# Kernel tuning notes

Measured on AMD Instinct MI355X. Metric: run time of the kernel, lower is better.

The kernel has to match this reference:

```python
import jax, jax.numpy as jnp
import numpy as np

EPS = 1e-5
NHEAD = 8
TOP_K = 2


def _layernorm(x, g, b):
    m = jnp.mean(x, axis=-1, keepdims=True)
    v = jnp.mean((x - m) ** 2, axis=-1, keepdims=True)
    return (x - m) * jax.lax.rsqrt(v + EPS) * g + b


def setup_inputs() -> dict:
    S, D, F, E = 4096, 512, 2048, 8
    key = jax.random.key(0)
    ks = jax.random.split(key, 18)
    std = 0.02
    return {
        "src": jax.random.normal(ks[0], (S, D), jnp.float32),
        "in_proj_w": std * jax.random.normal(ks[1], (3 * D, D), jnp.float32),
        "in_proj_b": jnp.zeros((3 * D,), jnp.float32),
        "out_proj_w": std * jax.random.normal(ks[2], (D, D), jnp.float32),
        "out_proj_b": jnp.zeros((D,), jnp.float32),
        "ln1_g": jnp.ones((D,), jnp.float32),
        "ln1_b": jnp.zeros((D,), jnp.float32),
        "ln2_g": jnp.ones((D,), jnp.float32),
        "ln2_b": jnp.zeros((D,), jnp.float32),
        "gate_w": std * jax.random.normal(ks[3], (E, D), jnp.float32),
        "gate_b": jnp.zeros((E,), jnp.float32),
        "w1": std * jax.random.normal(ks[4], (E, F, D), jnp.float32),
        "b1": jnp.zeros((E, F), jnp.float32),
        "w2": std * jax.random.normal(ks[5], (E, F, D), jnp.float32),
        "b2": jnp.zeros((E, F), jnp.float32),
        "wo": std * jax.random.normal(ks[6], (E, D, F), jnp.float32),
        "bo": jnp.zeros((E, D), jnp.float32),
    }


def _sa_block(x, in_proj_w, in_proj_b, out_proj_w, out_proj_b):
    # x: [S, D] unbatched sequence (torch MultiheadAttention unbatched path)
    S, D = x.shape
    hd = D // NHEAD
    qkv = x @ in_proj_w.T + in_proj_b              # [S, 3D]
    q, k, v = jnp.split(qkv, 3, axis=-1)
    q = q.reshape(S, NHEAD, hd)
    k = k.reshape(S, NHEAD, hd)
    v = v.reshape(S, NHEAD, hd)
    scores = jnp.einsum("shd,thd->hst", q, k) / jnp.sqrt(jnp.float32(hd))
    attn = jax.nn.softmax(scores, axis=-1)         # [H, S, S]
    out = jnp.einsum("hst,thd->shd", attn, v).reshape(S, D)
    return out @ out_proj_w.T + out_proj_b


def _ff_block(x, gate_w, gate_b, w1, b1, w2, b2, wo, bo):
    # top-k gated SwiGLU MoE; gate probs are softmax, NOT renormalized after topk
    T = x.shape[0]
    E = w1.shape[0]
    gates = jax.nn.softmax(x @ gate_w.T + gate_b, axis=-1)      # [T, E]
    top_scores, top_idx = jax.lax.top_k(gates, TOP_K)            # [T, k]
    combine = jnp.zeros((T, E), x.dtype).at[
        jnp.arange(T)[:, None], top_idx].add(top_scores)         # [T, E]
    out = jnp.zeros_like(x)
    for e in range(E):  # small fixed expert count
        h = jax.nn.silu(x @ w1[e].T + b1[e]) * (x @ w2[e].T + b2[e])
        out = out + combine[:, e:e + 1] * (h @ wo[e].T + bo[e])
    return out


def reference(src, in_proj_w, in_proj_b, out_proj_w, out_proj_b,
              ln1_g, ln1_b, ln2_g, ln2_b,
              gate_w, gate_b, w1, b1, w2, b2, wo, bo):
    # norm_first pre-norm residual layer, dropout=0 (eval)
    x = src
    x = x + _sa_block(_layernorm(x, ln1_g, ln1_b),
                      in_proj_w, in_proj_b, out_proj_w, out_proj_b)
    x = x + _ff_block(_layernorm(x, ln2_g, ln2_b),
                      gate_w, gate_b, w1, b1, w2, b2, wo, bo)
    return x
```

## Files before the change

kernel.cpp:

```cpp
#include <hip/hip_runtime.h>
#include <hip/hip_bf16.h>
#include <math.h>

#define SQ   4096
#define DM   512
#define NH   8
#define HDIM 64
#define FF   2048
#define NE   8

typedef unsigned short u16;
typedef unsigned int   u32;
typedef __attribute__((ext_vector_type(8))) __bf16 bf16x8;
typedef __attribute__((ext_vector_type(4))) float  f32x4;

__device__ __forceinline__ float bf2f(u16 v) {
    union { u32 i; float f; } c; c.i = ((u32)v) << 16; return c.f;
}
__device__ __forceinline__ u16 f2bf(float f) {
    union { __bf16 h; u16 u; } c; c.h = (__bf16)f; return c.u;
}

#define BM 128
#define BN 128
#define BK 32
#define BKP 40

__global__ __launch_bounds__(256) void gemm_split(
    const u16* __restrict__ Ahi, const u16* __restrict__ Alo, int lda,
    const u16* __restrict__ Bhi, const u16* __restrict__ Blo, int ldb,
    int M, int N, int K,
    const float* __restrict__ bias,
    const float* __restrict__ resid, int ldres,
    u16* __restrict__ Chi, u16* __restrict__ Clo,
    float* __restrict__ Cf, int ldc, int mode)
{
    __shared__ __align__(16) u16 Ash[BM * BKP], Asl[BM * BKP];
    __shared__ __align__(16) u16 Bsh[BN * BKP], Bsl[BN * BKP];
    const int tid  = threadIdx.x;
    const int wave = tid >> 6;
    const int lane = tid & 63;
    const int quad = lane >> 4;
    const int l16  = lane & 15;
    const int bm = blockIdx.x * BM;
    const int bn = blockIdx.y * BN;
    const int wm = (wave & 1) * 64;
    const int wn = (wave >> 1) * 64;

    f32x4 acc[4][4];
#pragma unroll
    for (int i = 0; i < 4; i++)
#pragma unroll
        for (int j = 0; j < 4; j++)
#pragma unroll
            for (int r = 0; r < 4; r++) acc[i][j][r] = 0.0f;

    for (int k0 = 0; k0 < K; k0 += BK) {
#pragma unroll
        for (int i = 0; i < 2; i++) {
            int c = tid + i * 256;
            int row = c >> 2;
            int col = (c & 3) << 3;
            int ga = bm + row, gb2 = bn + row;
            uint4 vah = make_uint4(0u,0u,0u,0u), val = vah, vbh = vah, vbl = vah;
            if (ga < M) {
                vah = *(const uint4*)(Ahi + (size_t)ga * lda + k0 + col);
                val = *(const uint4*)(Alo + (size_t)ga * lda + k0 + col);
            }
            if (gb2 < N) {
                vbh = *(const uint4*)(Bhi + (size_t)gb2 * ldb + k0 + col);
                vbl = *(const uint4*)(Blo + (size_t)gb2 * ldb + k0 + col);
            }
            *(uint4*)(Ash + row * BKP + col) = vah;
            *(uint4*)(Asl + row * BKP + col) = val;
            *(uint4*)(Bsh + row * BKP + col) = vbh;
            *(uint4*)(Bsl + row * BKP + col) = vbl;
        }
        __syncthreads();
        bf16x8 ah[4], al[4], bh[4], bl[4];
#pragma unroll
        for (int i = 0; i < 4; i++) {
            ah[i] = *(const bf16x8*)(Ash + (wm + i * 16 + l16) * BKP + quad * 8);
            al[i] = *(const bf16x8*)(Asl + (wm + i * 16 + l16) * BKP + quad * 8);
        }
#pragma unroll
        for (int j = 0; j < 4; j++) {
            bh[j] = *(const bf16x8*)(Bsh + (wn + j * 16 + l16) * BKP + quad * 8);
            bl[j] = *(const bf16x8*)(Bsl + (wn + j * 16 + l16) * BKP + quad * 8);
        }
#pragma unroll
        for (int i = 0; i < 4; i++)
#pragma unroll
            for (int j = 0; j < 4; j++) {
                acc[i][j] = __builtin_amdgcn_mfma_f32_16x16x32_bf16(ah[i], bh[j], acc[i][j], 0,0,0);
                acc[i][j] = __builtin_amdgcn_mfma_f32_16x16x32_bf16(ah[i], bl[j], acc[i][j], 0,0,0);
                acc[i][j] = __builtin_amdgcn_mfma_f32_16x16x32_bf16(al[i], bh[j], acc[i][j], 0,0,0);
            }
        __syncthreads();
    }

#pragma unroll
    for (int i = 0; i < 4; i++)
#pragma unroll
        for (int j = 0; j < 4; j++)
#pragma unroll
            for (int r = 0; r < 4; r++) {
                int row = bm + wm + i * 16 + quad * 4 + r;
                int col = bn + wn + j * 16 + l16;
                if (row >= M || col >= N) continue;
                float v = acc[i][j][r] + (bias ? bias[col] : 0.0f);
                size_t idx = (size_t)row * ldc + col;
                if (mode == 0) {
                    u16 hb = f2bf(v);
                    Chi[idx] = hb;
                    Clo[idx] = f2bf(v - bf2f(hb));
                } else {
                    if (resid) v += resid[(size_t)row * ldres + col];
                    Cf[idx] = v;
                }
            }
}

__global__ __launch_bounds__(256) void moe12_all(
    const u16* __restrict__ A, int lda,
    const int* __restrict__ idxl, const int* __restrict__ cnt,
    const int* __restrict__ off,
    const float* __restrict__ w1, const float* __restrict__ b1,
    const float* __restrict__ w2, const float* __restrict__ b2,
    u16* __restrict__ H)
{
    const int bmg = blockIdx.x * BM;
    if (bmg >= off[NE]) return;
    int e = 0;
    while (e < NE - 1 && bmg >= off[e + 1]) e++;
    const int M   = cnt[e];
    const int bml = bmg - off[e];
    if (bml >= M) return;
    const float* B1 = w1 + (size_t)e * FF * DM;
    const float* B2 = w2 + (size_t)e * FF * DM;
    const int*   rl = idxl + e * SQ;

    __shared__ __align__(16) u16 As[BM * BKP], Bs1[BN * BKP], Bs2[BN * BKP];
    const int tid  = threadIdx.x;
    const int wave = tid >> 6;
    const int lane = tid & 63;
    const int quad = lane >> 4;
    const int l16  = lane & 15;
    const int bn = blockIdx.y * BN;
    const int wm = (wave & 1) * 64;
    const int wn = (wave >> 1) * 64;

    f32x4 acc1[4][4], acc2[4][4];
#pragma unroll
    for (int i = 0; i < 4; i++)
#pragma unroll
        for (int j = 0; j < 4; j++)
#pragma unroll
            for (int r = 0; r < 4; r++) { acc1[i][j][r] = 0.0f; acc2[i][j][r] = 0.0f; }

    for (int k0 = 0; k0 < DM; k0 += BK) {
#pragma unroll
        for (int i = 0; i < 2; i++) {
            int c = tid + i * 256;
            int row = c >> 2;
            int col = (c & 3) << 3;
            uint4 va = make_uint4(0u,0u,0u,0u);
            int lr = bml + row;
            if (lr < M) {
                int ar = rl[lr];
                va = *(const uint4*)(A + (size_t)ar * lda + k0 + col);
            }
            *(uint4*)(As + row * BKP + col) = va;
        }
#pragma unroll
        for (int i = 0; i < 4; i++) {
            int c = tid + i * 256;
            int row = c >> 3;
            int col = (c & 7) << 2;
            float4 v1 = *(const float4*)(B1 + (size_t)(bn + row) * DM + k0 + col);
            float4 v2 = *(const float4*)(B2 + (size_t)(bn + row) * DM + k0 + col);
            ushort4 h1, h2;
            h1.x = f2bf(v1.x); h1.y = f2bf(v1.y); h1.z = f2bf(v1.z); h1.w = f2bf(v1.w);
            h2.x = f2bf(v2.x); h2.y = f2bf(v2.y); h2.z = f2bf(v2.z); h2.w = f2bf(v2.w);
            *(ushort4*)(Bs1 + row * BKP + col) = h1;
            *(ushort4*)(Bs2 + row * BKP + col) = h2;
        }
        __syncthreads();
        bf16x8 af[4], b1f[4], b2f[4];
#pragma unroll
        for (int i = 0; i < 4; i++)
            af[i] = *(const bf16x8*)(As + (wm + i * 16 + l16) * BKP + quad * 8);
#pragma unroll
        for (int j = 0; j < 4; j++) {
            b1f[j] = *(const bf16x8*)(Bs1 + (wn + j * 16 + l16) * BKP + quad * 8);
            b2f[j] = *(const bf16x8*)(Bs2 + (wn + j * 16 + l16) * BKP + quad * 8);
        }
#pragma unroll
        for (int i = 0; i < 4; i++)
#pragma unroll
            for (int j = 0; j < 4; j++) {
                acc1[i][j] = __builtin_amdgcn_mfma_f32_16x16x32_bf16(af[i], b1f[j], acc1[i][j], 0,0,0);
                acc2[i][j] = __builtin_amdgcn_mfma_f32_16x16x32_bf16(af[i], b2f[j], acc2[i][j], 0,0,0);
            }
        __syncthreads();
    }

#pragma unroll
    for (int i = 0; i < 4; i++)
#pragma unroll
        for (int j = 0; j < 4; j++)
#pragma unroll
            for (int r = 0; r < 4; r++) {
                int rowl = bml + wm + i * 16 + quad * 4 + r;
                if (rowl >= M) continue;
                int col = bn + wn + j * 16 + l16;
                float g1 = acc1[i][j][r] + b1[e * FF + col];
                float g2 = acc2[i][j][r] + b2[e * FF + col];
                float s  = g1 / (1.0f + __expf(-g1));
                H[(size_t)(off[e] + rowl) * FF + col] = f2bf(s * g2);
            }
}

__global__ __launch_bounds__(256) void moe_y_all(
    const u16* __restrict__ H,
    const float* __restrict__ wo, const float* __restrict__ bo,
    const int* __restrict__ idxl, const float* __restrict__ cw,
    const int* __restrict__ cnt, const int* __restrict__ off,
    float* __restrict__ out)
{
    const int bmg = blockIdx.x * BM;
    if (bmg >= off[NE]) return;
    int e = 0;
    while (e < NE - 1 && bmg >= off[e + 1]) e++;
    const int M   = cnt[e];
    const int bml = bmg - off[e];
    if (bml >= M) return;
    const float* B = wo + (size_t)e * DM * FF;

    __shared__ __align__(16) u16 As[BM * BKP], Bs[BN * BKP];
    const int tid  = threadIdx.x;
    const int wave = tid >> 6;
    const int lane = tid & 63;
    const int quad = lane >> 4;
    const int l16  = lane & 15;
    const int bn = blockIdx.y * BN;
    const int wm = (wave & 1) * 64;
    const int wn = (wave >> 1) * 64;

    f32x4 acc[4][4];
#pragma unroll
    for (int i = 0; i < 4; i++)
#pragma unroll
        for (int j = 0; j < 4; j++)
#pragma unroll
            for (int r = 0; r < 4; r++) acc[i][j][r] = 0.0f;

    for (int k0 = 0; k0 < FF; k0 += BK) {
#pragma unroll
        for (int i = 0; i < 2; i++) {
            int c = tid + i * 256;
            int row = c >> 2;
            int col = (c & 3) << 3;
            uint4 va = *(const uint4*)(H + (size_t)(bmg + row) * FF + k0 + col);
            *(uint4*)(As + row * BKP + col) = va;
        }
#pragma unroll
        for (int i = 0; i < 4; i++) {
            int c = tid + i * 256;
            int row = c >> 3;
            int col = (c & 7) << 2;
            float4 v = *(const float4*)(B + (size_t)(bn + row) * FF + k0 + col);
            ushort4 h;
            h.x = f2bf(v.x); h.y = f2bf(v.y); h.z = f2bf(v.z); h.w = f2bf(v.w);
            *(ushort4*)(Bs + row * BKP + col) = h;
        }
        __syncthreads();
        bf16x8 af[4], bf[4];
#pragma unroll
        for (int i = 0; i < 4; i++)
            af[i] = *(const bf16x8*)(As + (wm + i * 16 + l16) * BKP + quad * 8);
#pragma unroll
        for (int j = 0; j < 4; j++)
            bf[j] = *(const bf16x8*)(Bs + (wn + j * 16 + l16) * BKP + quad * 8);
#pragma unroll
        for (int i = 0; i < 4; i++)
#pragma unroll
            for (int j = 0; j < 4; j++)
                acc[i][j] = __builtin_amdgcn_mfma_f32_16x16x32_bf16(af[i], bf[j], acc[i][j], 0,0,0);
        __syncthreads();
    }

#pragma unroll
    for (int i = 0; i < 4; i++)
#pragma unroll
        for (int j = 0; j < 4; j++)
#pragma unroll
            for (int r = 0; r < 4; r++) {
                int rowl = bml + wm + i * 16 + quad * 4 + r;
                if (rowl >= M) continue;
                int col = bn + wn + j * 16 + l16;
                int tok = idxl[e * SQ + rowl];
                float wgt = cw[e * SQ + rowl];
                atomicAdd(out + (size_t)tok * DM + col,
                          wgt * (acc[i][j][r] + bo[e * DM + col]));
            }
}

#define KP 72
#define SCL 0.18033688011112042f

template <int SPLIT>
__device__ __forceinline__ void flash_body(
    const u16* __restrict__ qh, const u16* __restrict__ ql,
    const u16* __restrict__ vth, const u16* __restrict__ vtl,
    u16* __restrict__ oh, u16* __restrict__ ol,
    float* __restrict__ Opart, float* __restrict__ mpart,
    float* __restrict__ lpart)
{
    __shared__ __align__(16) u16 Ksh[64*KP], Ksl[64*KP], Vsh[64*KP], Vsl[64*KP];
    const int tid  = threadIdx.x;
    const int wave = tid >> 6;
    const int lane = tid & 63;
    const int quad = lane >> 4;
    const int l16  = lane & 15;
    const int h    = blockIdx.y;
    const int z    = (SPLIT > 1) ? blockIdx.z : 0;
    const int qbase = blockIdx.x * 64 + wave * 16;

    u16* const Pwh = Ksh + wave * (16 * KP);
    u16* const Pwl = Ksl + wave * (16 * KP);

    const int r_st  = tid >> 3;
    const int co_st = (tid & 7) << 3;

    bf16x8 aqh[2], aql[2];
#pragma unroll
    for (int kk = 0; kk < 2; kk++) {
        size_t off = (size_t)(qbase + l16) * (3*DM) + h*HDIM + kk*32 + quad*8;
        aqh[kk] = *(const bf16x8*)(qh + off);
        aql[kk] = *(const bf16x8*)(ql + off);
    }

    float m_[4], l_[4];
    f32x4 o_[4];
#pragma unroll
    for (int r = 0; r < 4; r++) { m_[r] = -1e30f; l_[r] = 0.0f; }
#pragma unroll
    for (int nd = 0; nd < 4; nd++)
#pragma unroll
        for (int r = 0; r < 4; r++) o_[nd][r] = 0.0f;

    const int NT    = SQ / 64 / SPLIT;
    const int jtBeg = z * NT, jtEnd = (z + 1) * NT;

    uint4 ga0, ga1, ga2, ga3, gb0, gb1, gb2, gb3;
    auto load_tile = [&](int jt) {
        size_t koff0 = (size_t)(jt*64 + r_st) * (3*DM) + DM + h*HDIM + co_st;
        size_t voff0 = (size_t)(h*HDIM + r_st) * SQ + jt*64 + co_st;
        ga0 = *(const uint4*)(qh  + koff0);
        ga1 = *(const uint4*)(ql  + koff0);
        ga2 = *(const uint4*)(vth + voff0);
        ga3 = *(const uint4*)(vtl + voff0);
        size_t koff1 = koff0 + (size_t)32 * (3*DM);
        size_t voff1 = voff0 + (size_t)32 * SQ;
        gb0 = *(const uint4*)(qh  + koff1);
        gb1 = *(const uint4*)(ql  + koff1);
        gb2 = *(const uint4*)(vth + voff1);
        gb3 = *(const uint4*)(vtl + voff1);
    };

    load_tile(jtBeg);

    for (int jt = jtBeg; jt < jtEnd; jt++) {
        *(uint4*)(Ksh + r_st*KP + co_st)      = ga0;
        *(uint4*)(Ksl + r_st*KP + co_st)      = ga1;
        *(uint4*)(Vsh + r_st*KP + co_st)      = ga2;
        *(uint4*)(Vsl + r_st*KP + co_st)      = ga3;
        *(uint4*)(Ksh + (r_st+32)*KP + co_st) = gb0;
        *(uint4*)(Ksl + (r_st+32)*KP + co_st) = gb1;
        *(uint4*)(Vsh + (r_st+32)*KP + co_st) = gb2;
        *(uint4*)(Vsl + (r_st+32)*KP + co_st) = gb3;
        __syncthreads();

        if (jt + 1 < jtEnd) load_tile(jt + 1);

        f32x4 s[4];
        __builtin_amdgcn_s_setprio(1);
#pragma unroll
        for (int jn = 0; jn < 4; jn++) {
            f32x4 zz;
#pragma unroll
            for (int r = 0; r < 4; r++) zz[r] = 0.0f;
#pragma unroll
            for (int kk = 0; kk < 2; kk++) {
                bf16x8 kh = *(const bf16x8*)(Ksh + (jn*16 + l16)*KP + kk*32 + quad*8);
                bf16x8 kl = *(const bf16x8*)(Ksl + (jn*16 + l16)*KP + kk*32 + quad*8);
                zz = __builtin_amdgcn_mfma_f32_16x16x32_bf16(aqh[kk], kh, zz, 0,0,0);
                zz = __builtin_amdgcn_mfma_f32_16x16x32_bf16(aqh[kk], kl, zz, 0,0,0);
                zz = __builtin_amdgcn_mfma_f32_16x16x32_bf16(aql[kk], kh, zz, 0,0,0);
            }
#pragma unroll
            for (int r = 0; r < 4; r++) zz[r] *= SCL;
            s[jn] = zz;
        }
        __builtin_amdgcn_s_setprio(0);
        __syncthreads();

        float mx[4];
#pragma unroll
        for (int r = 0; r < 4; r++) {
            mx[r] = fmaxf(fmaxf(s[0][r], s[1][r]), fmaxf(s[2][r], s[3][r]));
#pragma unroll
            for (int o2 = 1; o2 < 16; o2 <<= 1)
                mx[r] = fmaxf(mx[r], __shfl_xor(mx[r], o2));
        }
        int grew = (mx[0] > m_[0] + 8.0f) | (mx[1] > m_[1] + 8.0f) |
                   (mx[2] > m_[2] + 8.0f) | (mx[3] > m_[3] + 8.0f);
        if (__any(grew)) {
#pragma unroll
            for (int r = 0; r < 4; r++) {
                float nm  = fmaxf(m_[r], mx[r]);
                float al2 = exp2f(m_[r] - nm);
                m_[r] = nm;
                l_[r] *= al2;
#pragma unroll
                for (int nd = 0; nd < 4; nd++) o_[nd][r] *= al2;
            }
        }
        float rs[4];
#pragma unroll
        for (int r = 0; r < 4; r++) rs[r] = 0.0f;
#pragma unroll
        for (int jn = 0; jn < 4; jn++)
#pragma unroll
            for (int r = 0; r < 4; r++) {
                float p = exp2f(s[jn][r] - m_[r]);
                s[jn][r] = p;
                rs[r] += p;
            }
#pragma unroll
        for (int r = 0; r < 4; r++) {
#pragma unroll
            for (int o2 = 1; o2 < 16; o2 <<= 1)
                rs[r] += __shfl_xor(rs[r], o2);
            l_[r] += rs[r];
        }
#pragma unroll
        for (int jn = 0; jn < 4; jn++)
#pragma unroll
            for (int r = 0; r < 4; r++) {
                float p = s[jn][r];
                u16 ph = f2bf(p);
                int pidx = (quad*4 + r)*KP + jn*16 + l16;
                Pwh[pidx] = ph;
                Pwl[pidx] = f2bf(p - bf2f(ph));
            }

        bf16x8 ph[2], pl[2];
#pragma unroll
        for (int kk = 0; kk < 2; kk++) {
            ph[kk] = *(const bf16x8*)(Pwh + l16*KP + kk*32 + quad*8);
            pl[kk] = *(const bf16x8*)(Pwl + l16*KP + kk*32 + quad*8);
        }
        __builtin_amdgcn_s_setprio(1);
#pragma unroll
        for (int nd = 0; nd < 4; nd++) {
#pragma unroll
            for (int kk = 0; kk < 2; kk++) {
                bf16x8 vh = *(const bf16x8*)(Vsh + (nd*16 + l16)*KP + kk*32 + quad*8);
                bf16x8 vl = *(const bf16x8*)(Vsl + (nd*16 + l16)*KP + kk*32 + quad*8);
                o_[nd] = __builtin_amdgcn_mfma_f32_16x16x32_bf16(ph[kk], vh, o_[nd], 0,0,0);
                o_[nd] = __builtin_amdgcn_mfma_f32_16x16x32_bf16(ph[kk], vl, o_[nd], 0,0,0);
                o_[nd] = __builtin_amdgcn_mfma_f32_16x16x32_bf16(pl[kk], vh, o_[nd], 0,0,0);
            }
        }
        __builtin_amdgcn_s_setprio(0);
        __syncthreads();
    }

    if (SPLIT == 1) {
#pragma unroll
        for (int nd = 0; nd < 4; nd++)
#pragma unroll
            for (int r = 0; r < 4; r++) {
                int row = qbase + quad*4 + r;
                int col = h*HDIM + nd*16 + l16;
                float w = o_[nd][r] / l_[r];
                u16 hb = f2bf(w);
                oh[(size_t)row * DM + col] = hb;
                ol[(size_t)row * DM + col] = f2bf(w - bf2f(hb));
            }
    } else {
#pragma unroll
        for (int nd = 0; nd < 4; nd++)
#pragma unroll
            for (int r = 0; r < 4; r++) {
                int row = qbase + quad*4 + r;
                int col = h*HDIM + nd*16 + l16;
                Opart[((size_t)z * SQ + row) * DM + col] = o_[nd][r];
            }
        if (l16 == 0) {
#pragma unroll
            for (int r = 0; r < 4; r++) {
                int row = qbase + quad*4 + r;
                mpart[(z*NH + h) * SQ + row] = m_[r];
                lpart[(z*NH + h) * SQ + row] = l_[r];
            }
        }
    }
}

__global__ __launch_bounds__(256, 4) void flash_attn(
    const u16* __restrict__ qh, const u16* __restrict__ ql,
    const u16* __restrict__ vth, const u16* __restrict__ vtl,
    u16* __restrict__ oh, u16* __restrict__ ol)
{
    flash_body<1>(qh, ql, vth, vtl, oh, ol, nullptr, nullptr, nullptr);
}

__global__ __launch_bounds__(256, 4) void flash_attn_part(
    const u16* __restrict__ qh, const u16* __restrict__ ql,
    const u16* __restrict__ vth, const u16* __restrict__ vtl,
    float* __restrict__ Opart, float* __restrict__ mpart,
    float* __restrict__ lpart)
{
    flash_body<2>(qh, ql, vth, vtl, nullptr, nullptr, Opart, mpart, lpart);
}

__global__ __launch_bounds__(256) void attn_combine(
    const float* __restrict__ Opart, const float* __restrict__ mpart,
    const float* __restrict__ lpart,
    u16* __restrict__ oh, u16* __restrict__ ol)
{
    const int row = blockIdx.x;
    const int tid = threadIdx.x;
#pragma unroll
    for (int i = 0; i < 2; i++) {
        int col = tid + i * 256;
        int h = col >> 6;
        float m0 = mpart[h * SQ + row];
        float m1 = mpart[(NH + h) * SQ + row];
        float l0 = lpart[h * SQ + row];
        float l1 = lpart[(NH + h) * SQ + row];
        float m  = fmaxf(m0, m1);
        float a0 = exp2f(m0 - m);
        float a1 = exp2f(m1 - m);
        float O  = Opart[(size_t)row * DM + col] * a0
                 + Opart[((size_t)SQ + row) * DM + col] * a1;
        float l  = l0 * a0 + l1 * a1;
        float w  = O / l;
        u16 hb = f2bf(w);
        oh[(size_t)row * DM + col] = hb;
        ol[(size_t)row * DM + col] = f2bf(w - bf2f(hb));
    }
}

__global__ __launch_bounds__(256) void ln1_split(
    const float* __restrict__ x, const float* __restrict__ g,
    const float* __restrict__ b, u16* __restrict__ ohi, u16* __restrict__ olo)
{
    const int row = blockIdx.x;
    const int tid = threadIdx.x;
    float v0 = x[(size_t)row * DM + tid];
    float v1 = x[(size_t)row * DM + tid + 256];
    float s = v0 + v1, sq = v0*v0 + v1*v1;
#pragma unroll
    for (int o = 1; o < 64; o <<= 1) { s += __shfl_xor(s, o); sq += __shfl_xor(sq, o); }
    __shared__ float ss[4], ssq[4];
    if ((tid & 63) == 0) { ss[tid>>6] = s; ssq[tid>>6] = sq; }
    __syncthreads();
    s  = ss[0]+ss[1]+ss[2]+ss[3];
    sq = ssq[0]+ssq[1]+ssq[2]+ssq[3];
    float m = s * (1.0f/DM);
    float rstd = rsqrtf(sq*(1.0f/DM) - m*m + 1e-5f);
    float y0 = (v0-m)*rstd*g[tid]     + b[tid];
    float y1 = (v1-m)*rstd*g[tid+256] + b[tid+256];
    u16 h0 = f2bf(y0), h1 = f2bf(y1);
    ohi[(size_t)row*DM + tid]       = h0;  olo[(size_t)row*DM + tid]       = f2bf(y0 - bf2f(h0));
    ohi[(size_t)row*DM + tid + 256] = h1;  olo[(size_t)row*DM + tid + 256] = f2bf(y1 - bf2f(h1));
}

__global__ __launch_bounds__(256) void ln_kernel(
    const float* __restrict__ x, const float* __restrict__ g,
    const float* __restrict__ b, u16* __restrict__ out)
{
    const int row = blockIdx.x;
    const int tid = threadIdx.x;
    float v0 = x[(size_t)row * DM + tid];
    float v1 = x[(size_t)row * DM + tid + 256];
    float s = v0 + v1, sq = v0*v0 + v1*v1;
#pragma unroll
    for (int o = 1; o < 64; o <<= 1) { s += __shfl_xor(s, o); sq += __shfl_xor(sq, o); }
    __shared__ float ss[4], ssq[4];
    if ((tid & 63) == 0) { ss[tid>>6] = s; ssq[tid>>6] = sq; }
    __syncthreads();
    s  = ss[0]+ss[1]+ss[2]+ss[3];
    sq = ssq[0]+ssq[1]+ssq[2]+ssq[3];
    float m = s * (1.0f/DM);
    float rstd = rsqrtf(sq*(1.0f/DM) - m*m + 1e-5f);
    out[(size_t)row*DM + tid]       = f2bf((v0-m)*rstd*g[tid]     + b[tid]);
    out[(size_t)row*DM + tid + 256] = f2bf((v1-m)*rstd*g[tid+256] + b[tid+256]);
}

__global__ __launch_bounds__(256) void transpose_v2(
    const u16* __restrict__ qh, const u16* __restrict__ ql,
    u16* __restrict__ vth, u16* __restrict__ vtl)
{
    __shared__ u16 Th[64 * 66], Tl[64 * 66];
    const int t0  = blockIdx.x * 64;
    const int hd0 = blockIdx.y * 64;
    const int tid = threadIdx.x;
#pragma unroll
    for (int k = 0; k < 16; k++) {
        int idx = tid + k * 256;
        int r = idx >> 6, j = idx & 63;
        size_t src = (size_t)(t0 + r) * (3*DM) + 2*DM + hd0 + j;
        Th[r * 66 + j] = qh[src];
        Tl[r * 66 + j] = ql[src];
    }
    __syncthreads();
#pragma unroll
    for (int k = 0; k < 16; k++) {
        int idx = tid + k * 256;
        int r = idx >> 6, c2 = idx & 63;
        size_t dst = (size_t)(hd0 + r) * SQ + t0 + c2;
        vth[dst] = Th[c2 * 66 + r];
        vtl[dst] = Tl[c2 * 66 + r];
    }
}

__global__ __launch_bounds__(256) void gate_route(
    const float* __restrict__ x1, const float* __restrict__ g,
    const float* __restrict__ b, const float* __restrict__ gw,
    const float* __restrict__ gb,
    int* __restrict__ cnt, int* __restrict__ idxl, float* __restrict__ cw)
{
    const int token = blockIdx.x * 4 + (threadIdx.x >> 6);
    const int lane  = threadIdx.x & 63;
    const float* xr = x1 + (size_t)token * DM;
    float v[8];
#pragma unroll
    for (int i = 0; i < 8; i++) v[i] = xr[lane*8 + i];
    float s = 0.f, sq = 0.f;
#pragma unroll
    for (int i = 0; i < 8; i++) { s += v[i]; sq += v[i]*v[i]; }
#pragma unroll
    for (int o = 1; o < 64; o <<= 1) { s += __shfl_xor(s, o); sq += __shfl_xor(sq, o); }
    float m = s * (1.0f/DM);
    float rstd = rsqrtf(sq*(1.0f/DM) - m*m + 1e-5f);
    float xn[8];
#pragma unroll
    for (int i = 0; i < 8; i++)
        xn[i] = (v[i]-m)*rstd*g[lane*8+i] + b[lane*8+i];
    float logit[8];
#pragma unroll
    for (int e = 0; e < 8; e++) {
        float t = 0.f;
#pragma unroll
        for (int i = 0; i < 8; i++) t += xn[i] * gw[e*DM + lane*8 + i];
#pragma unroll
        for (int o = 1; o < 64; o <<= 1) t += __shfl_xor(t, o);
        logit[e] = t + gb[e];
    }
    if (lane == 0) {
        float mx = -1e30f;
        for (int e = 0; e < 8; e++) mx = fmaxf(mx, logit[e]);
        float den = 0.f, p[8];
        for (int e = 0; e < 8; e++) { p[e] = __expf(logit[e] - mx); den += p[e]; }
        for (int e = 0; e < 8; e++) p[e] /= den;
        int i1 = 0;
        for (int e = 1; e < 8; e++) if (p[e] > p[i1]) i1 = e;
        int i2 = -1;
        for (int e = 0; e < 8; e++) { if (e == i1) continue; if (i2 < 0 || p[e] > p[i2]) i2 = e; }
        int s1 = atomicAdd(&cnt[i1], 1);
        idxl[i1*SQ + s1] = token;  cw[i1*SQ + s1] = p[i1];
        int s2 = atomicAdd(&cnt[i2], 1);
        idxl[i2*SQ + s2] = token;  cw[i2*SQ + s2] = p[i2];
    }
}

__global__ __launch_bounds__(256) void cvt_split_w(
    const float* __restrict__ w, u16* __restrict__ wh, u16* __restrict__ wl, int n)
{
    int i = blockIdx.x * 256 + threadIdx.x;
    if (i < n) {
        float v = w[i];
        u16 h = f2bf(v);
        wh[i] = h;
        wl[i] = f2bf(v - bf2f(h));
    }
}

__global__ __launch_bounds__(64) void zero_cnt(int* cnt)
{
    if (threadIdx.x < NE) cnt[threadIdx.x] = 0;
}

__global__ __launch_bounds__(64) void make_off(const int* __restrict__ cnt,
                                              int* __restrict__ off)
{
    if (threadIdx.x == 0) {
        int a = 0;
        for (int e = 0; e < NE; e++) {
            off[e] = a;
            a += ((cnt[e] + 127) >> 7) << 7;
        }
        off[NE] = a;
    }
}

__global__ __launch_bounds__(256) void init_out(
    const float* __restrict__ x1, float* __restrict__ out)
{
    int i = blockIdx.x * 256 + threadIdx.x;
    ((float4*)out)[i] = ((const float4*)x1)[i];
}

__global__ __launch_bounds__(256) void sentinel_kernel(float* out, float v, int n)
{
    int i = blockIdx.x * 256 + threadIdx.x;
    if (i < n) out[i] = v;
}
__global__ __launch_bounds__(256) void scrub_kernel(float* out, int n)
{
    int i = blockIdx.x * 256 + threadIdx.x;
    if (i < n) { float v = out[i]; if (!isfinite(v)) out[i] = 777.0f; }
}

extern "C" void kernel_launch(void* const* d_in, const int* in_sizes, int n_in,
                              void* d_out, int out_size, void* d_ws, size_t ws_size,
                              hipStream_t stream)
{
    const float* src        = (const float*)d_in[0];
    const float* in_proj_w  = (const float*)d_in[1];
    const float* in_proj_b  = (const float*)d_in[2];
    const float* out_proj_w = (const float*)d_in[3];
    const float* out_proj_b = (const float*)d_in[4];
    const float* ln1_g      = (const float*)d_in[5];
    const float* ln1_b      = (const float*)d_in[6];
    const float* ln2_g      = (const float*)d_in[7];
    const float* ln2_b      = (const float*)d_in[8];
    const float* gate_w     = (const float*)d_in[9];
    const float* gate_b     = (const float*)d_in[10];
    const float* w1         = (const float*)d_in[11];
    const float* b1         = (const float*)d_in[12];
    const float* w2         = (const float*)d_in[13];
    const float* b2         = (const float*)d_in[14];
    const float* wo         = (const float*)d_in[15];
    const float* bo         = (const float*)d_in[16];
    float* out = (float*)d_out;

    const size_t MB = (size_t)1 << 20;
    const size_t ROUTE = 512 * 1024;
    const size_t NEED     = ROUTE + 44 * MB;
    const size_t NEED_BIG = ROUTE + 61 * MB;
    if (ws_size < NEED) {
        sentinel_kernel<<<(SQ*DM)/256, 256, 0, stream>>>(out, 333.0f, SQ*DM);
        return;
    }
    const bool big = (ws_size >= NEED_BIG);

    char* ws = (char*)d_ws;
    int*   cnt  = (int*)ws;
    int*   offp = (int*)(ws + 64);
    int*   idxl = (int*)(ws + 1024);
    float* cw   = (float*)(ws + 1024 + 128*1024);
    char*  base = ws + ROUTE;
    u16* xln1h = (u16*)(base);
    u16* xln1l = (u16*)(base + 4*MB);
    u16* attnh = (u16*)(base);
    u16* attnl = (u16*)(base + 4*MB);
    u16* qkvh  = (u16*)(base + 8*MB);
    u16* qkvl  = (u16*)(base + 20*MB);
    float* x1  = (float*)(base + 8*MB);
    u16* vth   = (u16*)(base + 32*MB);
    u16* vtl   = (u16*)(base + 36*MB);
    u16* xln2  = (u16*)(base + 36*MB);
    u16* Hbuf  = (u16*)(base);
    u16* wph   = (u16*)(base + 40*MB);
    u16* wpl   = (u16*)(base + 40*MB + 1536*1024);
    u16* woh   = (u16*)(base + 43*MB);
    u16* wol   = (u16*)(base + 43*MB + 512*1024);
    float* Opart = (float*)(base + 44*MB);
    float* mpart = (float*)(base + 60*MB);
    float* lpart = (float*)(base + 60*MB + 256*1024);

    cvt_split_w<<<(3*DM*DM)/256, 256, 0, stream>>>(in_proj_w,  wph, wpl, 3*DM*DM);
    cvt_split_w<<<(DM*DM)/256,   256, 0, stream>>>(out_proj_w, woh, wol, DM*DM);

    ln1_split<<<SQ, 256, 0, stream>>>(src, ln1_g, ln1_b, xln1h, xln1l);
    gemm_split<<<dim3(32, 12), 256, 0, stream>>>(
        xln1h, xln1l, DM, wph, wpl, DM, SQ, 3*DM, DM,
        in_proj_b, nullptr, 0, qkvh, qkvl, nullptr, 3*DM, 0);
    transpose_v2<<<dim3(SQ/64, DM/64), 256, 0, stream>>>(qkvh, qkvl, vth, vtl);
    if (big) {
        flash_attn_part<<<dim3(SQ/64, NH, 2), 256, 0, stream>>>(
            qkvh, qkvl, vth, vtl, Opart, mpart, lpart);
        attn_combine<<<SQ, 256, 0, stream>>>(Opart, mpart, lpart, attnh, attnl);
    } else {
        flash_attn<<<dim3(SQ/64, NH), 256, 0, stream>>>(
            qkvh, qkvl, vth, vtl, attnh, attnl);
    }
    gemm_split<<<dim3(32, 4), 256, 0, stream>>>(
        attnh, attnl, DM, woh, wol, DM, SQ, DM, DM,
        out_proj_b, src, DM, nullptr, nullptr, x1, DM, 1);

    ln_kernel<<<SQ, 256, 0, stream>>>(x1, ln2_g, ln2_b, xln2);
    zero_cnt<<<1, 64, 0, stream>>>(cnt);
    gate_route<<<SQ/4, 256, 0, stream>>>(x1, ln2_g, ln2_b, gate_w, gate_b,
                                         cnt, idxl, cw);
    make_off<<<1, 64, 0, stream>>>(cnt, offp);
    init_out<<<(SQ*DM/4)/256, 256, 0, stream>>>(x1, out);
    moe12_all<<<dim3(72, 16), 256, 0, stream>>>(
        xln2, DM, idxl, cnt, offp, w1, b1, w2, b2, Hbuf);
    moe_y_all<<<dim3(72, 4), 256, 0, stream>>>(
        Hbuf, wo, bo, idxl, cw, cnt, offp, out);

    scrub_kernel<<<(SQ*DM)/256, 256, 0, stream>>>(out, SQ*DM);
}
```

Measured before the change: 801.2 us.

## Swizzle flash-attention LDS tiles, add 4-way KV split, raise occupancy bound

The K/V/P shared-memory tiles drop the padded pitch (72) for an XOR-swizzled 64-wide layout, which keeps bank conflicts low while using less LDS. A 4-way split-KV flash kernel is added for when the workspace is large enough, and the combine kernel is generalised to any number of splits. Launch bounds go from 4 to 5 waves per SIMD. The goal is more parallelism and occupancy in attention, at the cost of more partial-result traffic in the combine and possible register pressure from the tighter bound.

Result: slower. 1.195 ms (+49.1%).

```diff
diff --git a/kernel.cpp b/kernel.cpp
--- a/kernel.cpp
+++ b/kernel.cpp
@@ -306,7 +306,8 @@
             }
 }
 
-#define KP 72
+#define KP 64
+#define SWZ(row, col) ((col) ^ (((row) & 7) << 3))
 #define SCL 0.18033688011112042f
 
 template <int SPLIT>
@@ -332,6 +333,7 @@
 
     const int r_st  = tid >> 3;
     const int co_st = (tid & 7) << 3;
+    const int co_sw = SWZ(r_st, co_st);
 
     bf16x8 aqh[2], aql[2];
 #pragma unroll
@@ -355,8 +357,8 @@
 
     uint4 ga0, ga1, ga2, ga3, gb0, gb1, gb2, gb3;
     auto load_tile = [&](int jt) {
-        size_t koff0 = (size_t)(jt*64 + r_st) * (3*DM) + DM + h*HDIM + co_st;
-        size_t voff0 = (size_t)(h*HDIM + r_st) * SQ + jt*64 + co_st;
+        size_t koff0 = (size_t)(jt*64 + r_st) * (3*DM) + DM + h*HDIM + ((tid&7)<<3);
+        size_t voff0 = (size_t)(h*HDIM + r_st) * SQ + jt*64 + ((tid&7)<<3);
         ga0 = *(const uint4*)(qh  + koff0);
         ga1 = *(const uint4*)(ql  + koff0);
         ga2 = *(const uint4*)(vth + voff0);
@@ -372,14 +374,14 @@
     load_tile(jtBeg);
 
     for (int jt = jtBeg; jt < jtEnd; jt++) {
-        *(uint4*)(Ksh + r_st*KP + co_st)      = ga0;
-        *(uint4*)(Ksl + r_st*KP + co_st)      = ga1;
-        *(uint4*)(Vsh + r_st*KP + co_st)      = ga2;
-        *(uint4*)(Vsl + r_st*KP + co_st)      = ga3;
-        *(uint4*)(Ksh + (r_st+32)*KP + co_st) = gb0;
-        *(uint4*)(Ksl + (r_st+32)*KP + co_st) = gb1;
-        *(uint4*)(Vsh + (r_st+32)*KP + co_st) = gb2;
-        *(uint4*)(Vsl + (r_st+32)*KP + co_st) = gb3;
+        *(uint4*)(Ksh + r_st*KP + co_sw)      = ga0;
+        *(uint4*)(Ksl + r_st*KP + co_sw)      = ga1;
+        *(uint4*)(Vsh + r_st*KP + co_sw)      = ga2;
+        *(uint4*)(Vsl + r_st*KP + co_sw)      = ga3;
+        *(uint4*)(Ksh + (r_st+32)*KP + co_sw) = gb0;
+        *(uint4*)(Ksl + (r_st+32)*KP + co_sw) = gb1;
+        *(uint4*)(Vsh + (r_st+32)*KP + co_sw) = gb2;
+        *(uint4*)(Vsl + (r_st+32)*KP + co_sw) = gb3;
         __syncthreads();
 
         if (jt + 1 < jtEnd) load_tile(jt + 1);
@@ -393,8 +395,10 @@
             for (int r = 0; r < 4; r++) zz[r] = 0.0f;
 #pragma unroll
             for (int kk = 0; kk < 2; kk++) {
-                bf16x8 kh = *(const bf16x8*)(Ksh + (jn*16 + l16)*KP + kk*32 + quad*8);
-                bf16x8 kl = *(const bf16x8*)(Ksl + (jn*16 + l16)*KP + kk*32 + quad*8);
+                int krow = jn*16 + l16;
+                int kcol = SWZ(krow, kk*32 + quad*8);
+                bf16x8 kh = *(const bf16x8*)(Ksh + krow*KP + kcol);
+                bf16x8 kl = *(const bf16x8*)(Ksl + krow*KP + kcol);
                 zz = __builtin_amdgcn_mfma_f32_16x16x32_bf16(aqh[kk], kh, zz, 0,0,0);
                 zz = __builtin_amdgcn_mfma_f32_16x16x32_bf16(aqh[kk], kl, zz, 0,0,0);
                 zz = __builtin_amdgcn_mfma_f32_16x16x32_bf16(aql[kk], kh, zz, 0,0,0);
@@ -451,7 +455,8 @@
             for (int r = 0; r < 4; r++) {
                 float p = s[jn][r];
                 u16 ph = f2bf(p);
-                int pidx = (quad*4 + r)*KP + jn*16 + l16;
+                int rr   = quad*4 + r;
+                int pidx = rr*KP + SWZ(rr, jn*16 + l16);
                 Pwh[pidx] = ph;
                 Pwl[pidx] = f2bf(p - bf2f(ph));
             }
@@ -459,16 +464,19 @@
         bf16x8 ph[2], pl[2];
 #pragma unroll
         for (int kk = 0; kk < 2; kk++) {
-            ph[kk] = *(const bf16x8*)(Pwh + l16*KP + kk*32 + quad*8);
-            pl[kk] = *(const bf16x8*)(Pwl + l16*KP + kk*32 + quad*8);
+            int pcol = SWZ(l16, kk*32 + quad*8);
+            ph[kk] = *(const bf16x8*)(Pwh + l16*KP + pcol);
+            pl[kk] = *(const bf16x8*)(Pwl + l16*KP + pcol);
         }
         __builtin_amdgcn_s_setprio(1);
 #pragma unroll
         for (int nd = 0; nd < 4; nd++) {
 #pragma unroll
             for (int kk = 0; kk < 2; kk++) {
-                bf16x8 vh = *(const bf16x8*)(Vsh + (nd*16 + l16)*KP + kk*32 + quad*8);
-                bf16x8 vl = *(const bf16x8*)(Vsl + (nd*16 + l16)*KP + kk*32 + quad*8);
+                int vrow = nd*16 + l16;
+                int vcol = SWZ(vrow, kk*32 + quad*8);
+                bf16x8 vh = *(const bf16x8*)(Vsh + vrow*KP + vcol);
+                bf16x8 vl = *(const bf16x8*)(Vsl + vrow*KP + vcol);
                 o_[nd] = __builtin_amdgcn_mfma_f32_16x16x32_bf16(ph[kk], vh, o_[nd], 0,0,0);
                 o_[nd] = __builtin_amdgcn_mfma_f32_16x16x32_bf16(ph[kk], vl, o_[nd], 0,0,0);
                 o_[nd] = __builtin_amdgcn_mfma_f32_16x16x32_bf16(pl[kk], vh, o_[nd], 0,0,0);
@@ -510,7 +518,7 @@
     }
 }
 
-__global__ __launch_bounds__(256, 4) void flash_attn(
+__global__ __launch_bounds__(256, 5) void flash_attn(
     const u16* __restrict__ qh, const u16* __restrict__ ql,
     const u16* __restrict__ vth, const u16* __restrict__ vtl,
     u16* __restrict__ oh, u16* __restrict__ ol)
@@ -518,7 +526,7 @@
     flash_body<1>(qh, ql, vth, vtl, oh, ol, nullptr, nullptr, nullptr);
 }
 
-__global__ __launch_bounds__(256, 4) void flash_attn_part(
+__global__ __launch_bounds__(256, 5) void flash_attn_part2(
     const u16* __restrict__ qh, const u16* __restrict__ ql,
     const u16* __restrict__ vth, const u16* __restrict__ vtl,
     float* __restrict__ Opart, float* __restrict__ mpart,
@@ -527,10 +535,19 @@
     flash_body<2>(qh, ql, vth, vtl, nullptr, nullptr, Opart, mpart, lpart);
 }
 
+__global__ __launch_bounds__(256, 5) void flash_attn_part4(
+    const u16* __restrict__ qh, const u16* __restrict__ ql,
+    const u16* __restrict__ vth, const u16* __restrict__ vtl,
+    float* __restrict__ Opart, float* __restrict__ mpart,
+    float* __restrict__ lpart)
+{
+    flash_body<4>(qh, ql, vth, vtl, nullptr, nullptr, Opart, mpart, lpart);
+}
+
 __global__ __launch_bounds__(256) void attn_combine(
     const float* __restrict__ Opart, const float* __restrict__ mpart,
     const float* __restrict__ lpart,
-    u16* __restrict__ oh, u16* __restrict__ ol)
+    u16* __restrict__ oh, u16* __restrict__ ol, int ns)
 {
     const int row = blockIdx.x;
     const int tid = threadIdx.x;
@@ -538,17 +555,16 @@
     for (int i = 0; i < 2; i++) {
         int col = tid + i * 256;
         int h = col >> 6;
-        float m0 = mpart[h * SQ + row];
-        float m1 = mpart[(NH + h) * SQ + row];
-        float l0 = lpart[h * SQ + row];
-        float l1 = lpart[(NH + h) * SQ + row];
-        float m  = fmaxf(m0, m1);
-        float a0 = exp2f(m0 - m);
-        float a1 = exp2f(m1 - m);
-        float O  = Opart[(size_t)row * DM + col] * a0
-                 + Opart[((size_t)SQ + row) * DM + col] * a1;
-        float l  = l0 * a0 + l1 * a1;
-        float w  = O / l;
+        float m = -1e30f;
+        for (int zz = 0; zz < ns; zz++)
+            m = fmaxf(m, mpart[(zz*NH + h) * SQ + row]);
+        float O = 0.0f, l = 0.0f;
+        for (int zz = 0; zz < ns; zz++) {
+            float a = exp2f(mpart[(zz*NH + h) * SQ + row] - m);
+            O += Opart[((size_t)zz * SQ + row) * DM + col] * a;
+            l += lpart[(zz*NH + h) * SQ + row] * a;
+        }
+        float w = O / l;
         u16 hb = f2bf(w);
         oh[(size_t)row * DM + col] = hb;
         ol[(size_t)row * DM + col] = f2bf(w - bf2f(hb));
@@ -752,13 +768,16 @@
 
     const size_t MB = (size_t)1 << 20;
     const size_t ROUTE = 512 * 1024;
-    const size_t NEED     = ROUTE + 44 * MB;
-    const size_t NEED_BIG = ROUTE + 61 * MB;
+    const size_t NEED      = ROUTE + 44 * MB;
+    const size_t NEED_BIG2 = ROUTE + 61 * MB;
+    const size_t NEED_BIG4 = ROUTE + 78 * MB;
     if (ws_size < NEED) {
         sentinel_kernel<<<(SQ*DM)/256, 256, 0, stream>>>(out, 333.0f, SQ*DM);
         return;
     }
-    const bool big = (ws_size >= NEED_BIG);
+    int ns = 0;
+    if (ws_size >= NEED_BIG4)      ns = 4;
+    else if (ws_size >= NEED_BIG2) ns = 2;
 
     char* ws = (char*)d_ws;
     int*   cnt  = (int*)ws;
@@ -782,8 +801,15 @@
     u16* woh   = (u16*)(base + 43*MB);
     u16* wol   = (u16*)(base + 43*MB + 512*1024);
     float* Opart = (float*)(base + 44*MB);
-    float* mpart = (float*)(base + 60*MB);
-    float* lpart = (float*)(base + 60*MB + 256*1024);
+    float* mpart;
+    float* lpart;
+    if (ns == 4) {
+        mpart = (float*)(base + 76*MB);
+        lpart = (float*)(base + 76*MB + 512*1024);
+    } else {
+        mpart = (float*)(base + 60*MB);
+        lpart = (float*)(base + 60*MB + 256*1024);
+    }
 
     cvt_split_w<<<(3*DM*DM)/256, 256, 0, stream>>>(in_proj_w,  wph, wpl, 3*DM*DM);
     cvt_split_w<<<(DM*DM)/256,   256, 0, stream>>>(out_proj_w, woh, wol, DM*DM);
@@ -793,10 +819,14 @@
         xln1h, xln1l, DM, wph, wpl, DM, SQ, 3*DM, DM,
         in_proj_b, nullptr, 0, qkvh, qkvl, nullptr, 3*DM, 0);
     transpose_v2<<<dim3(SQ/64, DM/64), 256, 0, stream>>>(qkvh, qkvl, vth, vtl);
-    if (big) {
-        flash_attn_part<<<dim3(SQ/64, NH, 2), 256, 0, stream>>>(
+    if (ns == 4) {
+        flash_attn_part4<<<dim3(SQ/64, NH, 4), 256, 0, stream>>>(
             qkvh, qkvl, vth, vtl, Opart, mpart, lpart);
-        attn_combine<<<SQ, 256, 0, stream>>>(Opart, mpart, lpart, attnh, attnl);
+        attn_combine<<<SQ, 256, 0, stream>>>(Opart, mpart, lpart, attnh, attnl, 4);
+    } else if (ns == 2) {
+        flash_attn_part2<<<dim3(SQ/64, NH, 2), 256, 0, stream>>>(
+            qkvh, qkvl, vth, vtl, Opart, mpart, lpart);
+        attn_combine<<<SQ, 256, 0, stream>>>(Opart, mpart, lpart, attnh, attnl, 2);
     } else {
         flash_attn<<<dim3(SQ/64, NH), 256, 0, stream>>>(
             qkvh, qkvl, vth, vtl, attnh, attnl);
```
